# Optimization experiments

Measured on AMD Instinct MI355X. Metric: run time of the kernel, lower is better.

The kernel has to match this reference:

```python
import jax, jax.numpy as jnp
import numpy as np

B, G, H, K = 2, 16, 128, 8      # batch, grid side, hidden, edges per grid point
TG = B * G ** 3                  # total grid points = 8192
E = TG * K                       # total edges = 65536
N = 2048                         # total atoms
EPS = 1e-5


def _bn(x, g, b):
    # eval-mode BatchNorm3d with running_mean=0, running_var=1
    s = g / jnp.sqrt(1.0 + EPS)
    return x * s[None, :, None, None, None] + b[None, :, None, None, None]


def _conv(x, w, pad):
    return jax.lax.conv_general_dilated(
        x, w, window_strides=(1, 1, 1), padding=[(pad, pad)] * 3,
        dimension_numbers=("NCDHW", "OIDHW", "NCDHW"))


def _mlp2(x, w1, b1, w2, b2, act):
    return act(x @ w1 + b1) @ w2 + b2


def setup_inputs() -> dict:
    key = jax.random.key(0)
    ks = jax.random.split(key, 16)
    def nrm(k, shape, scale=1.0):
        return jax.random.normal(k, shape, dtype=jnp.float32) * scale
    def lin(k, i, o):
        return nrm(k, (i, o), 1.0 / np.sqrt(i))
    return {
        "node_embedding": nrm(ks[0], (N, H)),
        "node_pos": nrm(ks[1], (N, 3)),
        "grid_pos": nrm(ks[2], (TG, 3)),
        "edge_row": jax.random.randint(ks[3], (E,), 0, N),
        # every grid point covered K times -> bincount never zero (matches original's div-by-bincount)
        "edge_col": jnp.repeat(jnp.arange(TG), K),
        "edge_w1": lin(ks[4], 6, H),    "edge_b1": jnp.zeros(H),
        "edge_w2": lin(ks[5], H, H),    "edge_b2": jnp.zeros(H),
        "msg_w1": lin(ks[6], 2 * H, H), "msg_b1": jnp.zeros(H),
        "msg_w2": lin(ks[7], H, H),     "msg_b2": jnp.zeros(H),
        "upd_w1": lin(ks[8], H, H),     "upd_b1": jnp.zeros(H),
        "upd_w2": lin(ks[9], H, H),     "upd_b2": jnp.zeros(H),
        "in_gamma": jnp.ones(H), "in_beta": jnp.zeros(H),
        "blk_conv1": nrm(ks[10], (3, H, H, 3, 3, 3), 1.0 / np.sqrt(H * 27)),
        "blk_bn1_g": jnp.ones((3, H)), "blk_bn1_b": jnp.zeros((3, H)),
        "blk_conv2": nrm(ks[11], (3, H, H, 3, 3, 3), 1.0 / np.sqrt(H * 27)),
        "blk_bn2_g": jnp.ones((3, H)), "blk_bn2_b": jnp.zeros((3, H)),
        "blk_conv5": nrm(ks[12], (3, H, H, 5, 5, 5), 1.0 / np.sqrt(H * 125)),
        "blk_bns_g": jnp.ones((3, H)), "blk_bns_b": jnp.zeros((3, H)),
        "fc_w": lin(ks[13], H, 20), "fc_b": jnp.zeros(20),
    }


def reference(node_embedding, node_pos, grid_pos, edge_row, edge_col,
              edge_w1, edge_b1, edge_w2, edge_b2,
              msg_w1, msg_b1, msg_w2, msg_b2,
              upd_w1, upd_b1, upd_w2, upd_b2,
              in_gamma, in_beta,
              blk_conv1, blk_bn1_g, blk_bn1_b,
              blk_conv2, blk_bn2_g, blk_bn2_b,
              blk_conv5, blk_bns_g, blk_bns_b,
              fc_w, fc_b):
    silu = jax.nn.silu
    # ---- MPNN message: gather -> edge MLP -> message MLP ----
    edge_attr = jnp.concatenate([node_pos[edge_row], grid_pos[edge_col]], axis=-1)  # [E,6]
    pos_emb = _mlp2(edge_attr, edge_w1, edge_b1, edge_w2, edge_b2, silu)            # [E,H]
    msg_in = jnp.concatenate([node_embedding[edge_row], pos_emb], axis=-1)          # [E,2H]
    message = _mlp2(msg_in, msg_w1, msg_b1, msg_w2, msg_b2, silu)                   # [E,H]
    # ---- scatter-mean onto grid points (global_add_pool / bincount) ----
    agg = jax.ops.segment_sum(message, edge_col, num_segments=TG)
    cnt = jax.ops.segment_sum(jnp.ones((E,), jnp.float32), edge_col, num_segments=TG)
    agg = agg / cnt[:, None]
    x = _mlp2(agg, upd_w1, upd_b1, upd_w2, upd_b2, silu)                            # [TG,H]
    # ---- to dense grid, channels-first ----
    x = x.reshape(B, G, G, G, H).transpose(0, 4, 1, 2, 3)                           # [B,H,G,G,G]
    x = _bn(x, in_gamma, in_beta)
    # ---- 3 residual blocks (eval BN, dropout identity) ----
    for i in range(3):
        left = jax.nn.relu(_bn(_conv(x, blk_conv1[i], 1), blk_bn1_g[i], blk_bn1_b[i]))
        left = _bn(_conv(left, blk_conv2[i], 1), blk_bn2_g[i], blk_bn2_b[i])
        short = _bn(_conv(x, blk_conv5[i], 2), blk_bns_g[i], blk_bns_b[i])
        x = jax.nn.relu(left + short)
    # ---- global max pool (kernel == spatial size) + fc + log_softmax ----
    pooled = x.max(axis=(2, 3, 4))                                                  # [B,H]
    logits = pooled @ fc_w + fc_b                                                   # [B,20]
    return jax.nn.log_softmax(logits, axis=-1)
```

## Files before the change

### kernel.cpp

```cpp
#include <hip/hip_runtime.h>
#include <math.h>


#define EPS_BN 1e-5f

typedef _Float16 f16x8 __attribute__((ext_vector_type(8)));
typedef float f32x4 __attribute__((ext_vector_type(4)));

struct us4 { unsigned short x, y, z, w; };

__device__ __forceinline__ float silu_f(float x) {
  return x / (1.0f + __expf(-x));
}
__device__ __forceinline__ unsigned short f2h(float x) {
  union { _Float16 h; unsigned short u; } v; v.h = (_Float16)x; return v.u;
}
__device__ __forceinline__ float h2f(unsigned short u) {
  union { unsigned short u; _Float16 h; } v; v.u = u; return (float)v.h;
}

template<int AMODE, int KTOT>
__global__ __launch_bounds__(256, 2)
void gemm_k(const float* __restrict__ A,
            const float* __restrict__ emb,
            const int* __restrict__ rows,
            const int* __restrict__ cols,
            const float* __restrict__ npos,
            const float* __restrict__ gpos,
            const float* __restrict__ ew1,
            const float* __restrict__ eb1,
            const float* __restrict__ W,
            const float* __restrict__ bias,
            const float* __restrict__ pscale,
            const float* __restrict__ pshift,
            float* __restrict__ C,
            int act, int obf)
{
  __shared__ __align__(16) float As[32][68];
  __shared__ __align__(16) float Bs[32][128];
  const int t = threadIdx.x;
  const int mbase = blockIdx.x * 64;
  const int m0 = (t >> 4) << 2;
  const int nA = (t & 15) << 2;

  const int ml = t >> 2;
  const int ks = (t & 3) << 3;

  float acc[4][8];
#pragma unroll
  for (int i = 0; i < 4; i++)
#pragma unroll
    for (int j = 0; j < 8; j++) acc[i][j] = 0.f;

  float at0=0,at1=0,at2=0,at3=0,at4=0,at5=0;
  int rowm = 0;
  if (AMODE == 1) {
    const int e = mbase + ml;
    const int r = rows[e];
    const int g = cols[e];
    at0 = npos[r*3+0]; at1 = npos[r*3+1]; at2 = npos[r*3+2];
    at3 = gpos[g*3+0]; at4 = gpos[g*3+1]; at5 = gpos[g*3+2];
  } else if (AMODE == 2) {
    rowm = rows[mbase + ml];
  }

  for (int k0 = 0; k0 < KTOT; k0 += 32) {
    if (AMODE == 1) {
#pragma unroll
      for (int j = 0; j < 8; j++) {
        const int k = k0 + ks + j;
        float s = eb1[k];
        s = fmaf(at0, ew1[      k], s);
        s = fmaf(at1, ew1[128 + k], s);
        s = fmaf(at2, ew1[256 + k], s);
        s = fmaf(at3, ew1[384 + k], s);
        s = fmaf(at4, ew1[512 + k], s);
        s = fmaf(at5, ew1[640 + k], s);
        As[ks + j][ml] = silu_f(s);
      }
    } else {
      const float* src;
      if (AMODE == 2) {
        const int gk = k0 + ks;
        src = (gk < 128) ? (emb + (size_t)rowm * 128 + gk)
                         : (A + (size_t)(mbase + ml) * 128 + (gk - 128));
      } else {
        src = A + (size_t)(mbase + ml) * KTOT + (k0 + ks);
      }
      const float4 a0 = *(const float4*)src;
      const float4 a1 = *(const float4*)(src + 4);
      As[ks+0][ml]=a0.x; As[ks+1][ml]=a0.y; As[ks+2][ml]=a0.z; As[ks+3][ml]=a0.w;
      As[ks+4][ml]=a1.x; As[ks+5][ml]=a1.y; As[ks+6][ml]=a1.z; As[ks+7][ml]=a1.w;
    }
    {
      const int kl = t >> 3;
      const int ns = (t & 7) << 4;
      const float* wsrc = W + (size_t)(k0 + kl) * 128 + ns;
      const float4 w0 = *(const float4*)(wsrc + 0);
      const float4 w1 = *(const float4*)(wsrc + 4);
      const float4 w2 = *(const float4*)(wsrc + 8);
      const float4 w3 = *(const float4*)(wsrc + 12);
      *(float4*)&Bs[kl][ns +  0] = w0;
      *(float4*)&Bs[kl][ns +  4] = w1;
      *(float4*)&Bs[kl][ns +  8] = w2;
      *(float4*)&Bs[kl][ns + 12] = w3;
    }
    __syncthreads();
#pragma unroll 8
    for (int kk = 0; kk < 32; kk++) {
      const float4 av = *(const float4*)&As[kk][m0];
      const float4 b0 = *(const float4*)&Bs[kk][nA];
      const float4 b1 = *(const float4*)&Bs[kk][nA + 64];
      const float a[4]  = {av.x, av.y, av.z, av.w};
      const float bb[8] = {b0.x, b0.y, b0.z, b0.w, b1.x, b1.y, b1.z, b1.w};
#pragma unroll
      for (int i = 0; i < 4; i++)
#pragma unroll
        for (int j = 0; j < 8; j++)
          acc[i][j] = fmaf(a[i], bb[j], acc[i][j]);
    }
    __syncthreads();
  }

  const float rs = rsqrtf(1.f + EPS_BN);
#pragma unroll
  for (int i = 0; i < 4; i++) {
    const size_t row = (size_t)(mbase + m0 + i);
    float v[8];
#pragma unroll
    for (int j = 0; j < 8; j++) {
      const int col = (j < 4) ? (nA + j) : (nA + 60 + j);
      float x = acc[i][j] + bias[col];
      if (act == 1) x = silu_f(x);
      if (pscale) x = fmaf(x, pscale[col] * rs, pshift[col]);
      v[j] = x;
    }
    if (obf) {
      unsigned short* Cb = (unsigned short*)C;
      us4 r0, r1;
      r0.x=f2h(v[0]); r0.y=f2h(v[1]); r0.z=f2h(v[2]); r0.w=f2h(v[3]);
      r1.x=f2h(v[4]); r1.y=f2h(v[5]); r1.z=f2h(v[6]); r1.w=f2h(v[7]);
      *(us4*)&Cb[row * 128 + nA]      = r0;
      *(us4*)&Cb[row * 128 + nA + 64] = r1;
    } else {
      *(float4*)&C[row * 128 + nA]      = make_float4(v[0], v[1], v[2], v[3]);
      *(float4*)&C[row * 128 + nA + 64] = make_float4(v[4], v[5], v[6], v[7]);
    }
  }
}

__global__ __launch_bounds__(256)
void aggregate_k(const float* __restrict__ msg, float* __restrict__ agg)
{
  const int i = blockIdx.x * 256 + threadIdx.x;
  const int g = i >> 7;
  const int o = i & 127;
  float s = 0.f;
#pragma unroll
  for (int j = 0; j < 8; j++)
    s += msg[(size_t)((g << 3) + j) * 128 + o];
  agg[i] = s * 0.125f;
}

__global__ __launch_bounds__(256)
void wpack_k(const float* __restrict__ w, unsigned short* __restrict__ wp, int T)
{
  const int i = blockIdx.x * 256 + threadIdx.x;
  if (i >= 3 * 4 * 8 * 64 * 8) return;
  const int j  = i & 7;
  const int l  = (i >> 3) & 63;
  const int nt = (i >> 9) & 7;
  const int kq = (i >> 12) & 3;
  const int ib = i >> 14;
  const int o = nt * 16 + (l & 15);
  const int c = kq * 32 + (l >> 4) * 8 + j;
  const float* src = w + ((size_t)(ib * 128 + o) * 128 + c) * T;
  unsigned short* dst = wp + (size_t)(ib * T) * 16384
                           + (size_t)(kq * 8 + nt) * 512 + l * 8 + j;
  for (int tp = 0; tp < T; tp++)
    dst[(size_t)tp * 16384] = f2h(src[tp]);
}

template<int KS>
__global__ __launch_bounds__(256, 1)
void convmf_k(const unsigned short* __restrict__ xin,
              const unsigned short* __restrict__ wpack,
              float* __restrict__ part)
{
  constexpr int P  = KS / 2;
  constexpr int SW = 16 + 2 * P;
  __shared__ __align__(16) unsigned short Ab[4 * SW * 128];
  __shared__ __align__(16) unsigned short Bb[16384];

  const int t   = threadIdx.x;
  const int bx  = blockIdx.x;
  const int kd  = bx >> 7;
  const int rem = bx & 127;
  const int b   = rem >> 6;
  const int z   = (rem >> 2) & 15;
  const int y0  = (rem & 3) << 2;
  const int zz  = z + kd - P;
  float* pout = part + (size_t)kd * (8192 * 128);
  const size_t obase = ((size_t)((b * 16 + z) * 16 + y0) * 16) * 128;

  if ((unsigned)zz >= 16u) {
    float4 zf = make_float4(0, 0, 0, 0);
    float4* dst = (float4*)(pout + obase);
    for (int i = t; i < 2048; i += 256) dst[i] = zf;
    return;
  }

  const int l  = t & 63, w = t >> 6;
  const int lx = l & 15, lq = l >> 4;
  const int mb = (w >> 1) << 1;
  const int nb = (w & 1) << 2;

  f32x4 acc[2][4];
#pragma unroll
  for (int i = 0; i < 2; i++)
#pragma unroll
    for (int j = 0; j < 4; j++) acc[i][j] = (f32x4){0.f, 0.f, 0.f, 0.f};

  const unsigned short* inplane = xin + ((size_t)(b * 16 + zz) * 256) * 128;
  const unsigned short* wkd = wpack + (size_t)(kd * KS * KS) * 16384;

  for (int kh = 0; kh < KS; kh++) {
    __syncthreads();
    for (int idx = t; idx < 4 * SW * 16; idx += 256) {
      const int ry = idx / (SW * 16);
      const int r2 = idx - ry * (SW * 16);
      const int xs = r2 >> 4;
      const int u  = r2 & 15;
      const int y  = y0 + ry + kh - P;
      const int x  = xs - P;
      uint4 val = make_uint4(0, 0, 0, 0);
      if ((unsigned)y < 16u && (unsigned)x < 16u)
        val = *(const uint4*)(inplane + ((size_t)(y * 16 + x)) * 128 + u * 8);
      const int du = (ry * SW + xs) * 16 + (u ^ (xs & 7));
      *(uint4*)(Ab + (size_t)du * 8) = val;
    }
    const unsigned short* wkh = wkd + (size_t)(kh * KS) * 16384;
    for (int kw = 0; kw < KS; kw++) {
      __syncthreads();
      {
        const unsigned short* g = wkh + (size_t)kw * 16384 + t * 8;
        unsigned short* dl = Bb + t * 8;
#pragma unroll
        for (int r = 0; r < 8; r++) {
          __builtin_amdgcn_global_load_lds(
              (const __attribute__((address_space(1))) unsigned int*)(g + r * 2048),
              (__attribute__((address_space(3))) unsigned int*)(dl + r * 2048),
              16, 0, 0);
        }
      }
      __syncthreads();
      const int xsw = lx + kw;
      const int xm  = xsw & 7;
#pragma unroll
      for (int kq = 0; kq < 4; kq++) {
        f16x8 a0 = *(const f16x8*)(Ab + (size_t)(((mb + 0) * SW + xsw) * 16 + ((kq * 4 + lq) ^ xm)) * 8);
        f16x8 a1 = *(const f16x8*)(Ab + (size_t)(((mb + 1) * SW + xsw) * 16 + ((kq * 4 + lq) ^ xm)) * 8);
        const unsigned short* bbase = Bb + (size_t)((kq * 8 + nb) * 64 + l) * 8;
#pragma unroll
        for (int j = 0; j < 4; j++) {
          f16x8 bv = *(const f16x8*)(bbase + (size_t)j * 512);
          acc[0][j] = __builtin_amdgcn_mfma_f32_16x16x32_f16(a0, bv, acc[0][j], 0, 0, 0);
          acc[1][j] = __builtin_amdgcn_mfma_f32_16x16x32_f16(a1, bv, acc[1][j], 0, 0, 0);
        }
      }
    }
  }

#pragma unroll
  for (int i = 0; i < 2; i++) {
    const int my = mb + i;
#pragma unroll
    for (int r = 0; r < 4; r++) {
      const size_t vrow = obase + (size_t)(my * 16 + lq * 4 + r) * 128;
#pragma unroll
      for (int j = 0; j < 4; j++)
        pout[vrow + (nb + j) * 16 + lx] = acc[i][j][r];
    }
  }
}

__global__ __launch_bounds__(256)
void combine1_k(const float* __restrict__ p,
                const float* __restrict__ g, const float* __restrict__ be,
                unsigned short* __restrict__ o)
{
  const int i = blockIdx.x * 256 + threadIdx.x;
  const size_t off = (size_t)i * 4;
  const int c = (i & 31) * 4;
  float4 a0 = *(const float4*)(p + off);
  float4 a1 = *(const float4*)(p + 1048576 + off);
  float4 a2 = *(const float4*)(p + 2097152 + off);
  const float rs = rsqrtf(1.f + EPS_BN);
  float4 gg = *(const float4*)(g + c);
  float4 bb = *(const float4*)(be + c);
  float v0 = fmaxf(fmaf(a0.x + a1.x + a2.x, gg.x * rs, bb.x), 0.f);
  float v1 = fmaxf(fmaf(a0.y + a1.y + a2.y, gg.y * rs, bb.y), 0.f);
  float v2 = fmaxf(fmaf(a0.z + a1.z + a2.z, gg.z * rs, bb.z), 0.f);
  float v3 = fmaxf(fmaf(a0.w + a1.w + a2.w, gg.w * rs, bb.w), 0.f);
  us4 r; r.x = f2h(v0); r.y = f2h(v1); r.z = f2h(v2); r.w = f2h(v3);
  *(us4*)(o + off) = r;
}

__global__ __launch_bounds__(256)
void combine2_k(const float* __restrict__ p2, const float* __restrict__ p5,
                const float* __restrict__ g2, const float* __restrict__ b2,
                const float* __restrict__ gs, const float* __restrict__ bs,
                unsigned short* __restrict__ o)
{
  const int i = blockIdx.x * 256 + threadIdx.x;
  const size_t off = (size_t)i * 4;
  const int c = (i & 31) * 4;
  float4 s2 = *(const float4*)(p2 + off);
  {
    float4 a1 = *(const float4*)(p2 + 1048576 + off);
    float4 a2 = *(const float4*)(p2 + 2097152 + off);
    s2.x += a1.x + a2.x; s2.y += a1.y + a2.y;
    s2.z += a1.z + a2.z; s2.w += a1.w + a2.w;
  }
  float4 s5 = *(const float4*)(p5 + off);
#pragma unroll
  for (int gi = 1; gi < 5; gi++) {
    float4 a = *(const float4*)(p5 + (size_t)gi * 1048576 + off);
    s5.x += a.x; s5.y += a.y; s5.z += a.z; s5.w += a.w;
  }
  const float rs = rsqrtf(1.f + EPS_BN);
  float4 gg2 = *(const float4*)(g2 + c);
  float4 bb2 = *(const float4*)(b2 + c);
  float4 ggs = *(const float4*)(gs + c);
  float4 bbs = *(const float4*)(bs + c);
  float v0 = fmaxf(fmaf(s2.x, gg2.x * rs, bb2.x) + fmaf(s5.x, ggs.x * rs, bbs.x), 0.f);
  float v1 = fmaxf(fmaf(s2.y, gg2.y * rs, bb2.y) + fmaf(s5.y, ggs.y * rs, bbs.y), 0.f);
  float v2 = fmaxf(fmaf(s2.z, gg2.z * rs, bb2.z) + fmaf(s5.z, ggs.z * rs, bbs.z), 0.f);
  float v3 = fmaxf(fmaf(s2.w, gg2.w * rs, bb2.w) + fmaf(s5.w, ggs.w * rs, bbs.w), 0.f);
  us4 r; r.x = f2h(v0); r.y = f2h(v1); r.z = f2h(v2); r.w = f2h(v3);
  *(us4*)(o + off) = r;
}

__global__ __launch_bounds__(256)
void pool_partial_k(const unsigned short* __restrict__ xg, float* __restrict__ pmax)
{
  __shared__ float red[256];
  const int bz = blockIdx.x;
  const int t = threadIdx.x;
  const int c = t & 127;
  const int h = t >> 7;
  const unsigned short* base = xg + (size_t)bz * 256 * 128;
  float m = -3.4e38f;
  for (int i = 0; i < 128; i++)
    m = fmaxf(m, h2f(base[(size_t)(h * 128 + i) * 128 + c]));
  red[t] = m;
  __syncthreads();
  if (t < 128) pmax[bz * 128 + t] = fmaxf(red[t], red[t + 128]);
}

__global__ __launch_bounds__(256)
void final_k(const float* __restrict__ pmax,
             const float* __restrict__ fc_w,
             const float* __restrict__ fc_b,
             float* __restrict__ outp)
{
  __shared__ float pool[2][128];
  __shared__ float lg[2][20];
  const int t = threadIdx.x;
  const int b = t >> 7;
  const int c = t & 127;
  float m = -3.4e38f;
  for (int zi = 0; zi < 16; zi++)
    m = fmaxf(m, pmax[(b * 16 + zi) * 128 + c]);
  pool[b][c] = m;
  __syncthreads();
  if (t < 40) {
    const int bb = t / 20, j = t % 20;
    float l = fc_b[j];
    for (int cc = 0; cc < 128; cc++)
      l = fmaf(pool[bb][cc], fc_w[cc * 20 + j], l);
    lg[bb][j] = l;
  }
  __syncthreads();
  if (t < 2) {
    float mx = -3.4e38f;
    for (int j = 0; j < 20; j++) mx = fmaxf(mx, lg[t][j]);
    float s = 0.f;
    for (int j = 0; j < 20; j++) s += expf(lg[t][j] - mx);
    const float ls = mx + logf(s);
    for (int j = 0; j < 20; j++) outp[t * 20 + j] = lg[t][j] - ls;
  }
}

extern "C" void kernel_launch(void* const* d_in, const int* in_sizes, int n_in,
                              void* d_out, int out_size, void* d_ws, size_t ws_size,
                              hipStream_t stream) {
  (void)in_sizes; (void)n_in; (void)out_size; (void)ws_size;
  const float* node_embedding = (const float*)d_in[0];
  const float* node_pos  = (const float*)d_in[1];
  const float* grid_pos  = (const float*)d_in[2];
  const int*   edge_row  = (const int*)d_in[3];
  const int*   edge_col  = (const int*)d_in[4];
  const float* edge_w1   = (const float*)d_in[5];
  const float* edge_b1   = (const float*)d_in[6];
  const float* edge_w2   = (const float*)d_in[7];
  const float* edge_b2   = (const float*)d_in[8];
  const float* msg_w1    = (const float*)d_in[9];
  const float* msg_b1    = (const float*)d_in[10];
  const float* msg_w2    = (const float*)d_in[11];
  const float* msg_b2    = (const float*)d_in[12];
  const float* upd_w1    = (const float*)d_in[13];
  const float* upd_b1    = (const float*)d_in[14];
  const float* upd_w2    = (const float*)d_in[15];
  const float* upd_b2    = (const float*)d_in[16];
  const float* in_gamma  = (const float*)d_in[17];
  const float* in_beta   = (const float*)d_in[18];
  const float* blk_conv1 = (const float*)d_in[19];
  const float* blk_bn1_g = (const float*)d_in[20];
  const float* blk_bn1_b = (const float*)d_in[21];
  const float* blk_conv2 = (const float*)d_in[22];
  const float* blk_bn2_g = (const float*)d_in[23];
  const float* blk_bn2_b = (const float*)d_in[24];
  const float* blk_conv5 = (const float*)d_in[25];
  const float* blk_bns_g = (const float*)d_in[26];
  const float* blk_bns_b = (const float*)d_in[27];
  const float* fc_w      = (const float*)d_in[28];
  const float* fc_b      = (const float*)d_in[29];

  float* ws = (float*)d_ws;
  float* bufA = ws;
  float* bufB = ws + 8388608;
  unsigned short* wp31 = (unsigned short*)ws;
  unsigned short* wp32 = (unsigned short*)(ws + 663552);
  unsigned short* wp5  = (unsigned short*)(ws + 1327104);
  float* p1   = ws + 4400128;
  float* p2   = ws + 7545856;
  float* p5   = ws + 10691584;
  unsigned short* xg0 = (unsigned short*)(ws + 16000000);
  unsigned short* xg1 = (unsigned short*)(ws + 16524288);
  unsigned short* tg  = (unsigned short*)(ws + 17048576);
  float* agg  = ws + 17572864;
  float* u1   = ws + 18621440;
  float* pmax = ws + 19670016;
  float* outF = (float*)d_out;

  gemm_k<1, 128><<<1024, 256, 0, stream>>>(
      nullptr, nullptr, edge_row, edge_col, node_pos, grid_pos, edge_w1, edge_b1,
      edge_w2, edge_b2, nullptr, nullptr, bufA, 0, 0);
  gemm_k<2, 256><<<1024, 256, 0, stream>>>(
      bufA, node_embedding, edge_row, nullptr, nullptr, nullptr, nullptr, nullptr,
      msg_w1, msg_b1, nullptr, nullptr, bufB, 1, 0);
  gemm_k<0, 128><<<1024, 256, 0, stream>>>(
      bufB, nullptr, nullptr, nullptr, nullptr, nullptr, nullptr, nullptr,
      msg_w2, msg_b2, nullptr, nullptr, bufA, 0, 0);
  aggregate_k<<<4096, 256, 0, stream>>>(bufA, agg);

  wpack_k<<<192, 256, 0, stream>>>(blk_conv1, wp31, 27);
  wpack_k<<<192, 256, 0, stream>>>(blk_conv2, wp32, 27);
  wpack_k<<<192, 256, 0, stream>>>(blk_conv5, wp5, 125);

  gemm_k<0, 128><<<128, 256, 0, stream>>>(
      agg, nullptr, nullptr, nullptr, nullptr, nullptr, nullptr, nullptr,
      upd_w1, upd_b1, nullptr, nullptr, u1, 1, 0);
  gemm_k<0, 128><<<128, 256, 0, stream>>>(
      u1, nullptr, nullptr, nullptr, nullptr, nullptr, nullptr, nullptr,
      upd_w2, upd_b2, in_gamma, in_beta, (float*)xg0, 0, 1);

  const unsigned short* xin = xg0;
  unsigned short* xout = xg1;
  for (int i = 0; i < 3; i++) {
    convmf_k<3><<<384, 256, 0, stream>>>(xin, wp31 + (size_t)i * 27 * 16384, p1);
    combine1_k<<<1024, 256, 0, stream>>>(p1, blk_bn1_g + i * 128, blk_bn1_b + i * 128, tg);
    convmf_k<3><<<384, 256, 0, stream>>>(tg, wp32 + (size_t)i * 27 * 16384, p2);
    convmf_k<5><<<640, 256, 0, stream>>>(xin, wp5 + (size_t)i * 125 * 16384, p5);
    combine2_k<<<1024, 256, 0, stream>>>(p2, p5,
        blk_bn2_g + i * 128, blk_bn2_b + i * 128,
        blk_bns_g + i * 128, blk_bns_b + i * 128, xout);
    unsigned short* tmp = (unsigned short*)xin;
    xin = xout;
    xout = tmp;
  }

  pool_partial_k<<<32, 256, 0, stream>>>(xin, pmax);
  final_k<<<1, 256, 0, stream>>>(pmax, fc_w, fc_b, outF);
}
```

Baseline: 623.9 us.

## Move edge/message MLP GEMMs to fp16 MFMA and fuse aggregation

Replaces the three fp32 SIMT GEMMs of the edge and message MLPs with an fp16 MFMA kernel that uses pre-packed weight panels loaded to LDS via global_load_lds, and a swizzled A tile. Intermediate edge activations are stored as fp16, halving traffic, and the segment-mean aggregation is fused into the last GEMM's epilogue, removing a separate kernel. This adds conversion and packing kernels and lowers intermediate precision to fp16.

```diff
diff --git a/kernel.cpp b/kernel.cpp
--- a/kernel.cpp
+++ b/kernel.cpp
@@ -22,13 +22,6 @@
 template<int AMODE, int KTOT>
 __global__ __launch_bounds__(256, 2)
 void gemm_k(const float* __restrict__ A,
-            const float* __restrict__ emb,
-            const int* __restrict__ rows,
-            const int* __restrict__ cols,
-            const float* __restrict__ npos,
-            const float* __restrict__ gpos,
-            const float* __restrict__ ew1,
-            const float* __restrict__ eb1,
             const float* __restrict__ W,
             const float* __restrict__ bias,
             const float* __restrict__ pscale,
@@ -42,7 +35,6 @@
   const int mbase = blockIdx.x * 64;
   const int m0 = (t >> 4) << 2;
   const int nA = (t & 15) << 2;
-
   const int ml = t >> 2;
   const int ks = (t & 3) << 3;
 
@@ -52,41 +44,9 @@
 #pragma unroll
     for (int j = 0; j < 8; j++) acc[i][j] = 0.f;
 
-  float at0=0,at1=0,at2=0,at3=0,at4=0,at5=0;
-  int rowm = 0;
-  if (AMODE == 1) {
-    const int e = mbase + ml;
-    const int r = rows[e];
-    const int g = cols[e];
-    at0 = npos[r*3+0]; at1 = npos[r*3+1]; at2 = npos[r*3+2];
-    at3 = gpos[g*3+0]; at4 = gpos[g*3+1]; at5 = gpos[g*3+2];
-  } else if (AMODE == 2) {
-    rowm = rows[mbase + ml];
-  }
-
   for (int k0 = 0; k0 < KTOT; k0 += 32) {
-    if (AMODE == 1) {
-#pragma unroll
-      for (int j = 0; j < 8; j++) {
-        const int k = k0 + ks + j;
-        float s = eb1[k];
-        s = fmaf(at0, ew1[      k], s);
-        s = fmaf(at1, ew1[128 + k], s);
-        s = fmaf(at2, ew1[256 + k], s);
-        s = fmaf(at3, ew1[384 + k], s);
-        s = fmaf(at4, ew1[512 + k], s);
-        s = fmaf(at5, ew1[640 + k], s);
-        As[ks + j][ml] = silu_f(s);
-      }
-    } else {
-      const float* src;
-      if (AMODE == 2) {
-        const int gk = k0 + ks;
-        src = (gk < 128) ? (emb + (size_t)rowm * 128 + gk)
-                         : (A + (size_t)(mbase + ml) * 128 + (gk - 128));
-      } else {
-        src = A + (size_t)(mbase + ml) * KTOT + (k0 + ks);
-      }
+    {
+      const float* src = A + (size_t)(mbase + ml) * KTOT + (k0 + ks);
       const float4 a0 = *(const float4*)src;
       const float4 a1 = *(const float4*)(src + 4);
       As[ks+0][ml]=a0.x; As[ks+1][ml]=a0.y; As[ks+2][ml]=a0.z; As[ks+3][ml]=a0.w;
@@ -96,14 +56,10 @@
       const int kl = t >> 3;
       const int ns = (t & 7) << 4;
       const float* wsrc = W + (size_t)(k0 + kl) * 128 + ns;
-      const float4 w0 = *(const float4*)(wsrc + 0);
-      const float4 w1 = *(const float4*)(wsrc + 4);
-      const float4 w2 = *(const float4*)(wsrc + 8);
-      const float4 w3 = *(const float4*)(wsrc + 12);
-      *(float4*)&Bs[kl][ns +  0] = w0;
-      *(float4*)&Bs[kl][ns +  4] = w1;
-      *(float4*)&Bs[kl][ns +  8] = w2;
-      *(float4*)&Bs[kl][ns + 12] = w3;
+      *(float4*)&Bs[kl][ns +  0] = *(const float4*)(wsrc + 0);
+      *(float4*)&Bs[kl][ns +  4] = *(const float4*)(wsrc + 4);
+      *(float4*)&Bs[kl][ns +  8] = *(const float4*)(wsrc + 8);
+      *(float4*)&Bs[kl][ns + 12] = *(const float4*)(wsrc + 12);
     }
     __syncthreads();
 #pragma unroll 8
@@ -150,16 +106,167 @@
 }
 
 __global__ __launch_bounds__(256)
-void aggregate_k(const float* __restrict__ msg, float* __restrict__ agg)
+void wpack_g_k(const float* __restrict__ w, unsigned short* __restrict__ wp,
+               int total)
 {
   const int i = blockIdx.x * 256 + threadIdx.x;
-  const int g = i >> 7;
-  const int o = i & 127;
-  float s = 0.f;
-#pragma unroll
-  for (int j = 0; j < 8; j++)
-    s += msg[(size_t)((g << 3) + j) * 128 + o];
-  agg[i] = s * 0.125f;
+  if (i >= total) return;
+  const int j   = i & 7;
+  const int l   = (i >> 3) & 63;
+  const int nt  = (i >> 9) & 7;
+  const int kq  = (i >> 12) & 3;
+  const int tap = i >> 14;
+  const int k = tap * 128 + kq * 32 + (l >> 4) * 8 + j;
+  const int n = nt * 16 + (l & 15);
+  wp[i] = f2h(w[(size_t)k * 128 + n]);
+}
+
+__global__ __launch_bounds__(256)
+void cvt_k(const float* __restrict__ src, unsigned short* __restrict__ dst, int n)
+{
+  const int i = blockIdx.x * 256 + threadIdx.x;
+  if (i < n) dst[i] = f2h(src[i]);
+}
+
+template<int AMODE, int TAPS>
+__global__ __launch_bounds__(256)
+void mgemm_k(const unsigned short* __restrict__ A,
+             const unsigned short* __restrict__ emb16,
+             const int* __restrict__ rows,
+             const int* __restrict__ cols,
+             const float* __restrict__ npos,
+             const float* __restrict__ gpos,
+             const float* __restrict__ ew1,
+             const float* __restrict__ eb1,
+             const unsigned short* __restrict__ wpanel,
+             const float* __restrict__ bias,
+             unsigned short* __restrict__ C,
+             float* __restrict__ aggout,
+             int act)
+{
+  __shared__ __align__(16) unsigned short Ab[64 * 128];
+  __shared__ __align__(16) unsigned short Bb[16384];
+  const int t = threadIdx.x;
+  const int mbase = blockIdx.x * 64;
+  const int l = t & 63, w = t >> 6;
+  const int lx = l & 15, lq = l >> 4;
+  const int mb = (w >> 1) << 1;
+  const int nb = (w & 1) << 2;
+  const int rowl = t >> 2;
+  const int seg  = t & 3;
+
+  float at0=0,at1=0,at2=0,at3=0,at4=0,at5=0;
+  int rowm = 0;
+  if (AMODE == 1) {
+    const int e = mbase + rowl;
+    const int r = rows[e];
+    const int g = cols[e];
+    at0 = npos[r*3+0]; at1 = npos[r*3+1]; at2 = npos[r*3+2];
+    at3 = gpos[g*3+0]; at4 = gpos[g*3+1]; at5 = gpos[g*3+2];
+  } else if (AMODE == 2) {
+    rowm = rows[mbase + rowl];
+  }
+
+  f32x4 acc[2][4];
+#pragma unroll
+  for (int i = 0; i < 2; i++)
+#pragma unroll
+    for (int j = 0; j < 4; j++) acc[i][j] = (f32x4){0.f, 0.f, 0.f, 0.f};
+
+  for (int tap = 0; tap < TAPS; tap++) {
+    __syncthreads();
+    if (AMODE == 1) {
+#pragma unroll
+      for (int uu = 0; uu < 4; uu++) {
+        union { unsigned short h[8]; uint4 v; } pk;
+#pragma unroll
+        for (int jj = 0; jj < 8; jj++) {
+          const int k = seg * 32 + uu * 8 + jj;
+          float s = eb1[k];
+          s = fmaf(at0, ew1[      k], s);
+          s = fmaf(at1, ew1[128 + k], s);
+          s = fmaf(at2, ew1[256 + k], s);
+          s = fmaf(at3, ew1[384 + k], s);
+          s = fmaf(at4, ew1[512 + k], s);
+          s = fmaf(at5, ew1[640 + k], s);
+          pk.h[jj] = f2h(silu_f(s));
+        }
+        const int u = seg * 4 + uu;
+        *(uint4*)(Ab + (size_t)(rowl * 16 + (u ^ (rowl & 7))) * 8) = pk.v;
+      }
+    } else {
+      const unsigned short* src;
+      if (AMODE == 2) {
+        src = (tap == 0) ? (emb16 + (size_t)rowm * 128 + seg * 32)
+                         : (A + (size_t)(mbase + rowl) * 128 + seg * 32);
+      } else {
+        src = A + (size_t)(mbase + rowl) * 128 + seg * 32;
+      }
+#pragma unroll
+      for (int uu = 0; uu < 4; uu++) {
+        const uint4 v = *(const uint4*)(src + uu * 8);
+        const int u = seg * 4 + uu;
+        *(uint4*)(Ab + (size_t)(rowl * 16 + (u ^ (rowl & 7))) * 8) = v;
+      }
+    }
+    {
+      const unsigned short* g = wpanel + (size_t)tap * 16384 + t * 8;
+      unsigned short* dl = Bb + t * 8;
+#pragma unroll
+      for (int r = 0; r < 8; r++) {
+        __builtin_amdgcn_global_load_lds(
+            (const __attribute__((address_space(1))) unsigned int*)(g + r * 2048),
+            (__attribute__((address_space(3))) unsigned int*)(dl + r * 2048),
+            16, 0, 0);
+      }
+    }
+    __syncthreads();
+    const int xm = lx & 7;
+#pragma unroll
+    for (int kq = 0; kq < 4; kq++) {
+      f16x8 a0 = *(const f16x8*)(Ab + (size_t)(((mb + 0) * 16 + lx) * 16 + ((kq * 4 + lq) ^ xm)) * 8);
+      f16x8 a1 = *(const f16x8*)(Ab + (size_t)(((mb + 1) * 16 + lx) * 16 + ((kq * 4 + lq) ^ xm)) * 8);
+      const unsigned short* bbase = Bb + (size_t)((kq * 8 + nb) * 64 + l) * 8;
+#pragma unroll
+      for (int j = 0; j < 4; j++) {
+        f16x8 bv = *(const f16x8*)(bbase + (size_t)j * 512);
+        acc[0][j] = __builtin_amdgcn_mfma_f32_16x16x32_f16(a0, bv, acc[0][j], 0, 0, 0);
+        acc[1][j] = __builtin_amdgcn_mfma_f32_16x16x32_f16(a1, bv, acc[1][j], 0, 0, 0);
+      }
+    }
+  }
+
+  __syncthreads();
+#pragma unroll
+  for (int i = 0; i < 2; i++) {
+#pragma unroll
+    for (int r = 0; r < 4; r++) {
+      const int rowloc = (mb + i) * 16 + lq * 4 + r;
+#pragma unroll
+      for (int j = 0; j < 4; j++) {
+        const int col = (nb + j) * 16 + lx;
+        float x = acc[i][j][r] + bias[col];
+        if (act == 1) x = silu_f(x);
+        Ab[rowloc * 128 + col] = f2h(x);
+      }
+    }
+  }
+  __syncthreads();
+  if (aggout) {
+#pragma unroll
+    for (int q = t * 4; q < t * 4 + 4; q++) {
+      const int g = q >> 7, c = q & 127;
+      float s = 0.f;
+#pragma unroll
+      for (int r = 0; r < 8; r++) s += h2f(Ab[(g * 8 + r) * 128 + c]);
+      aggout[(size_t)((mbase >> 3) + g) * 128 + c] = s * 0.125f;
+    }
+  } else {
+    const size_t base = (size_t)(mbase + rowl) * 128 + seg * 32;
+#pragma unroll
+    for (int uu = 0; uu < 4; uu++)
+      *(uint4*)(C + base + uu * 8) = *(const uint4*)(Ab + rowl * 128 + seg * 32 + uu * 8);
+  }
 }
 
 __global__ __launch_bounds__(256)
@@ -428,8 +535,8 @@
   const float* fc_b      = (const float*)d_in[29];
 
   float* ws = (float*)d_ws;
-  float* bufA = ws;
-  float* bufB = ws + 8388608;
+  unsigned short* bufA = (unsigned short*)ws;
+  unsigned short* bufB = (unsigned short*)(ws + 4194304);
   unsigned short* wp31 = (unsigned short*)ws;
   unsigned short* wp32 = (unsigned short*)(ws + 663552);
   unsigned short* wp5  = (unsigned short*)(ws + 1327104);
@@ -442,29 +549,35 @@
   float* agg  = ws + 17572864;
   float* u1   = ws + 18621440;
   float* pmax = ws + 19670016;
+  unsigned short* emb16 = (unsigned short*)(ws + 19675136);
+  unsigned short* wg_e2 = (unsigned short*)(ws + 19806208);
+  unsigned short* wg_m1 = (unsigned short*)(ws + 19814400);
+  unsigned short* wg_m2 = (unsigned short*)(ws + 19830784);
   float* outF = (float*)d_out;
 
-  gemm_k<1, 128><<<1024, 256, 0, stream>>>(
+  cvt_k<<<1024, 256, 0, stream>>>(node_embedding, emb16, 2048 * 128);
+  wpack_g_k<<<64, 256, 0, stream>>>(edge_w2, wg_e2, 16384);
+  wpack_g_k<<<128, 256, 0, stream>>>(msg_w1, wg_m1, 32768);
+  wpack_g_k<<<64, 256, 0, stream>>>(msg_w2, wg_m2, 16384);
+
+  mgemm_k<1, 1><<<1024, 256, 0, stream>>>(
       nullptr, nullptr, edge_row, edge_col, node_pos, grid_pos, edge_w1, edge_b1,
-      edge_w2, edge_b2, nullptr, nullptr, bufA, 0, 0);
-  gemm_k<2, 256><<<1024, 256, 0, stream>>>(
-      bufA, node_embedding, edge_row, nullptr, nullptr, nullptr, nullptr, nullptr,
-      msg_w1, msg_b1, nullptr, nullptr, bufB, 1, 0);
-  gemm_k<0, 128><<<1024, 256, 0, stream>>>(
+      wg_e2, edge_b2, bufA, nullptr, 0);
+  mgemm_k<2, 2><<<1024, 256, 0, stream>>>(
+      bufA, emb16, edge_row, nullptr, nullptr, nullptr, nullptr, nullptr,
+      wg_m1, msg_b1, bufB, nullptr, 1);
+  mgemm_k<0, 1><<<1024, 256, 0, stream>>>(
       bufB, nullptr, nullptr, nullptr, nullptr, nullptr, nullptr, nullptr,
-      msg_w2, msg_b2, nullptr, nullptr, bufA, 0, 0);
-  aggregate_k<<<4096, 256, 0, stream>>>(bufA, agg);
+      wg_m2, msg_b2, bufB, agg, 0);
 
   wpack_k<<<192, 256, 0, stream>>>(blk_conv1, wp31, 27);
   wpack_k<<<192, 256, 0, stream>>>(blk_conv2, wp32, 27);
   wpack_k<<<192, 256, 0, stream>>>(blk_conv5, wp5, 125);
 
   gemm_k<0, 128><<<128, 256, 0, stream>>>(
-      agg, nullptr, nullptr, nullptr, nullptr, nullptr, nullptr, nullptr,
-      upd_w1, upd_b1, nullptr, nullptr, u1, 1, 0);
+      agg, upd_w1, upd_b1, nullptr, nullptr, u1, 1, 0);
   gemm_k<0, 128><<<128, 256, 0, stream>>>(
-      u1, nullptr, nullptr, nullptr, nullptr, nullptr, nullptr, nullptr,
-      upd_w2, upd_b2, in_gamma, in_beta, (float*)xg0, 0, 1);
+      u1, upd_w2, upd_b2, in_gamma, in_beta, (float*)xg0, 0, 1);
 
   const unsigned short* xin = xg0;
   unsigned short* xout = xg1;
```

New measurement: 558.8 us. 1.12x faster.
